# Kernel tuning notes

Hardware: AMD Instinct MI355X
Metric: run time of the kernel (lower is better)

## Reference

```python
import jax, jax.numpy as jnp
import numpy as np

H, D = 16, 1024
HD = D // H  # 64

def setup_inputs() -> dict:
    key = jax.random.key(0)
    ks = jax.random.split(key, 11)
    B, S = 2, 2048
    s_in = 1.0 / np.sqrt(D)
    return {
        "V": jax.random.normal(ks[0], (B, S, D), jnp.float32),
        "K": jax.random.normal(ks[1], (B, S, D), jnp.float32),
        "Q": jax.random.normal(ks[2], (B, S, D), jnp.float32),
        # stacked per-head Linear weights, torch layout [out,in] -> [H, HD, D]
        "Wv": jax.random.normal(ks[3], (H, HD, D), jnp.float32) * s_in,
        "bv": jnp.zeros((H, HD), jnp.float32),
        "Wk": jax.random.normal(ks[4], (H, HD, D), jnp.float32) * s_in,
        "bk": jnp.zeros((H, HD), jnp.float32),
        "Wq": jax.random.normal(ks[5], (H, HD, D), jnp.float32) * s_in,
        "bq": jnp.zeros((H, HD), jnp.float32),
        "Wo": jax.random.normal(ks[6], (D, D), jnp.float32) * s_in,
        "bo": jnp.zeros((D,), jnp.float32),
    }

def reference(V, K, Q, Wv, bv, Wk, bk, Wq, bq, Wo, bo):
    scale = HD ** (-0.5)
    # per-head projections fused into one batched GEMM: [B,S,D] x [H,HD,D] -> [B,H,S,HD]
    q = jnp.einsum('bsd,hed->bhse', Q, Wq) + bq[None, :, None, :]
    k = jnp.einsum('bsd,hed->bhse', K, Wk) + bk[None, :, None, :]
    v = jnp.einsum('bsd,hed->bhse', V, Wv) + bv[None, :, None, :]
    # scaled dot-product attention
    scores = jnp.einsum('bhqe,bhke->bhqk', q, k) * scale  # [B,H,S,S]
    p = jax.nn.softmax(scores, axis=-1)
    att = jnp.einsum('bhqk,bhke->bhqe', p, v)  # [B,H,S,HD]
    # concat heads (head 0 first, matching the torch cat order) then output proj
    B, _, S, _ = att.shape
    cat = jnp.transpose(att, (0, 2, 1, 3)).reshape(B, S, H * HD)
    return cat @ Wo.T + bo
```

## Files before the change

kernel.cpp:

```cpp
#include <hip/hip_runtime.h>
#include <cstdint>
#include <cstddef>

typedef __bf16 bf16_t;
typedef bf16_t bf16x8 __attribute__((ext_vector_type(8)));
typedef bf16_t bf16x4 __attribute__((ext_vector_type(4)));
typedef float f32x4 __attribute__((ext_vector_type(4)));

__device__ __forceinline__ void gl_lds16(const void* g, void* l) {
  __builtin_amdgcn_global_load_lds(
      (const __attribute__((address_space(1))) void*)g,
      (__attribute__((address_space(3))) void*)l, 16, 0, 0);
}

__device__ __forceinline__ f32x4 mfma16(bf16x8 a, bf16x8 b, f32x4 c) {
  return __builtin_amdgcn_mfma_f32_16x16x32_bf16(a, b, c, 0, 0, 0);
}

#define SCHED_FENCE() __builtin_amdgcn_sched_barrier(0)
#define WAIT_VM0()   do { asm volatile("s_waitcnt vmcnt(0)");   SCHED_FENCE(); } while (0)
#define WAIT_LGKM0() do { asm volatile("s_waitcnt lgkmcnt(0)"); SCHED_FENCE(); } while (0)
#define RAW_BAR()    do { __builtin_amdgcn_s_barrier();         SCHED_FENCE(); } while (0)

struct CvtArgs { const float* src[7]; bf16_t* dst[7]; };

__global__ __launch_bounds__(256) void convert_all(CvtArgs a) {
  unsigned g = blockIdx.x * 256u + threadIdx.x;
  unsigned seg, off;
  if (g < 524288u) {
    seg = g >> 17; off = g & 131071u;
  } else {
    unsigned h = g - 524288u;
    seg = 4u + (h >> 19); off = h & 524287u;
  }
  const float4* s = (const float4*)a.src[seg] + (size_t)off * 2;
  float4 x0 = s[0], x1 = s[1];
  bf16x8 o;
  o[0] = (bf16_t)x0.x; o[1] = (bf16_t)x0.y; o[2] = (bf16_t)x0.z; o[3] = (bf16_t)x0.w;
  o[4] = (bf16_t)x1.x; o[5] = (bf16_t)x1.y; o[6] = (bf16_t)x1.z; o[7] = (bf16_t)x1.w;
  *(bf16x8*)(a.dst[seg] + (size_t)off * 8) = o;
}

__device__ __forceinline__ void stage128(const bf16_t* src, bf16_t* dst, int t, int w) {
  #pragma unroll
  for (int i = 0; i < 4; i++) {
    int g = t + i * 256;
    int r = g >> 3, pc = g & 7;
    int lc = pc ^ (r & 7);
    gl_lds16(src + (size_t)r * 1024 + lc * 8, dst + i * 2048 + w * 512);
  }
}
__device__ __forceinline__ void stage64(const bf16_t* src, bf16_t* dst, int t, int w) {
  #pragma unroll
  for (int i = 0; i < 2; i++) {
    int g = t + i * 256;
    int r = g >> 3, pc = g & 7;
    int lc = pc ^ (r & 7);
    gl_lds16(src + (size_t)r * 1024 + lc * 8, dst + i * 2048 + w * 512);
  }
}

struct ProjArgs {
  const bf16_t* A[3]; const bf16_t* W[3]; const float* bias[3];
  bf16_t* out[3]; float scale[3];
};

__global__ __launch_bounds__(256, 2) void gemm_proj(ProjArgs p) {
  __shared__ __attribute__((aligned(16))) unsigned char smem[65536];
  const int z = blockIdx.z;
  const bf16_t* A = p.A[z] + (size_t)blockIdx.x * 128 * 1024;
  const bf16_t* W = p.W[z] + (size_t)blockIdx.y * 128 * 1024;

  const int t = threadIdx.x;
  const int w = t >> 6, l = t & 63;
  const int lq = l >> 4, lr = l & 15;
  const int mq = w & 1, nq = w >> 1;

  f32x4 acc[4][4];
  f32x4 zero = {0.f, 0.f, 0.f, 0.f};
  #pragma unroll
  for (int i = 0; i < 4; i++)
    #pragma unroll
    for (int j = 0; j < 4; j++) acc[i][j] = zero;

  stage128(A, (bf16_t*)smem, t, w);
  stage128(W, (bf16_t*)(smem + 16384), t, w);
  WAIT_VM0();
  RAW_BAR();

  for (int step = 0; step < 16; ++step) {
    const int cur = step & 1;
    bf16_t* as = (bf16_t*)(smem + cur * 32768);
    bf16_t* bs = (bf16_t*)(smem + cur * 32768 + 16384);
    if (step < 15) {
      bf16_t* an = (bf16_t*)(smem + (cur ^ 1) * 32768);
      stage128(A + (step + 1) * 64, an, t, w);
      stage128(W + (step + 1) * 64, an + 8192, t, w);
    }
    SCHED_FENCE();
    #pragma unroll
    for (int kk = 0; kk < 2; kk++) {
      bf16x8 af[4], bfr[4];
      #pragma unroll
      for (int i = 0; i < 4; i++) {
        int R = mq * 64 + i * 16 + lr;
        int ch = (kk * 4 + lq) ^ (R & 7);
        af[i] = *(const bf16x8*)(as + R * 64 + ch * 8);
      }
      #pragma unroll
      for (int j = 0; j < 4; j++) {
        int R = nq * 64 + j * 16 + lr;
        int ch = (kk * 4 + lq) ^ (R & 7);
        bfr[j] = *(const bf16x8*)(bs + R * 64 + ch * 8);
      }
      __builtin_amdgcn_s_setprio(1);
      #pragma unroll
      for (int i = 0; i < 4; i++)
        #pragma unroll
        for (int j = 0; j < 4; j++)
          acc[i][j] = mfma16(af[i], bfr[j], acc[i][j]);
      __builtin_amdgcn_s_setprio(0);
    }
    WAIT_VM0();
    RAW_BAR();
  }

  const float* bias = p.bias[z];
  const float scale = p.scale[z];
  __syncthreads();
  bf16_t* ts = (bf16_t*)smem;
  #pragma unroll
  for (int i = 0; i < 4; i++) {
    #pragma unroll
    for (int j = 0; j < 4; j++) {
      int nl = nq * 64 + j * 16 + lr;
      float bz = bias[blockIdx.y * 128 + nl];
      #pragma unroll
      for (int r = 0; r < 4; r++) {
        int ml = mq * 64 + i * 16 + lq * 4 + r;
        bf16_t val = (bf16_t)((acc[i][j][r] + bz) * scale);
        if (z == 0) {
          int mlp = (ml & 96) | (((ml >> 2) & 3) << 3) | (((ml >> 4) & 1) << 2) | (ml & 3);
          ts[nl * 136 + mlp] = val;
        } else {
          ts[ml * 136 + nl] = val;
        }
      }
    }
  }
  __syncthreads();
  bf16_t* out = p.out[z];
  const int b = blockIdx.x >> 4, sbase = (blockIdx.x & 15) * 128;
  if (z == 0) {
    #pragma unroll
    for (int ii = 0; ii < 8; ii++) {
      int idx = t * 8 + ii * 2048;
      int rr = idx >> 7, cc = idx & 127;
      int n = blockIdx.y * 128 + rr;
      int h = n >> 6, e = n & 63;
      bf16x8 vq = *(const bf16x8*)(ts + rr * 136 + cc);
      *(bf16x8*)(out + ((size_t)(b * 16 + h) * 64 + e) * 2048 + sbase + cc) = vq;
    }
  } else {
    #pragma unroll
    for (int ii = 0; ii < 8; ii++) {
      int idx = t * 8 + ii * 2048;
      int rr = idx >> 7, cc = idx & 127;
      int n = blockIdx.y * 128 + cc;
      int h = n >> 6, e = n & 63;
      bf16x8 vq = *(const bf16x8*)(ts + rr * 136 + cc);
      *(bf16x8*)(out + ((size_t)(b * 16 + h) * 2048 + sbase + rr) * 64 + e) = vq;
    }
  }
}

__global__ __launch_bounds__(256, 4) void attn(
    const bf16_t* __restrict__ qw, const bf16_t* __restrict__ kw,
    const bf16_t* __restrict__ vtw, bf16_t* __restrict__ att)
{
  __shared__ __attribute__((aligned(16))) unsigned char smem[32768];
  bf16_t* qe_s = (bf16_t*)(smem + 16384);
  const int bh = blockIdx.x, qt = blockIdx.y;
  const int t = threadIdx.x, w = t >> 6, l = t & 63, lq = l >> 4, lr = l & 15;

  const bf16_t* kb0 = kw + (size_t)bh * 131072;
  const bf16_t* vb0 = vtw + (size_t)bh * 131072;

  const bf16_t* qbase = qw + ((size_t)bh * 2048 + qt * 64) * 64;
  #pragma unroll
  for (int i = 0; i < 2; i++) {
    int g = t + i * 256;
    int r = g >> 3, pc = g & 7;
    int lc = pc ^ (r & 7);
    gl_lds16(qbase + (size_t)r * 64 + lc * 8, qe_s + i * 2048 + w * 512);
    gl_lds16(kb0 + (size_t)r * 64 + lc * 8, (bf16_t*)smem + i * 2048 + w * 512);
    gl_lds16(vb0 + (size_t)r * 2048 + lc * 8, (bf16_t*)(smem + 8192) + i * 2048 + w * 512);
  }
  WAIT_VM0();
  RAW_BAR();
  bf16x8 qf[2];
  #pragma unroll
  for (int kk = 0; kk < 2; kk++) {
    int R = w * 16 + lr;
    int ch = (kk * 4 + lq) ^ (R & 7);
    qf[kk] = *(const bf16x8*)(qe_s + R * 64 + ch * 8);
  }
  WAIT_LGKM0();
  RAW_BAR();

  f32x4 O[4];
  f32x4 zero = {0.f, 0.f, 0.f, 0.f};
  #pragma unroll
  for (int et = 0; et < 4; et++) O[et] = zero;
  float lsum = 0.f;

  for (int kt = 0; kt < 32; ++kt) {
    const int cur = kt & 1;
    bf16_t* ks = (bf16_t*)(smem + cur * 16384);
    bf16_t* vs = (bf16_t*)(smem + cur * 16384 + 8192);
    if (kt < 31) {
      bf16_t* kn = (bf16_t*)(smem + (cur ^ 1) * 16384);
      const bf16_t* kbase = kb0 + (size_t)(kt + 1) * 64 * 64;
      const bf16_t* vbase = vb0 + (size_t)(kt + 1) * 64;
      #pragma unroll
      for (int i = 0; i < 2; i++) {
        int g = t + i * 256;
        int r = g >> 3, pc = g & 7;
        int lc = pc ^ (r & 7);
        gl_lds16(kbase + (size_t)r * 64 + lc * 8, kn + i * 2048 + w * 512);
        gl_lds16(vbase + (size_t)r * 2048 + lc * 8, kn + 4096 + i * 2048 + w * 512);
      }
    }
    SCHED_FENCE();

    f32x4 sc[4];
    #pragma unroll
    for (int j = 0; j < 4; j++) sc[j] = zero;
    #pragma unroll
    for (int kk = 0; kk < 2; kk++) {
      #pragma unroll
      for (int j = 0; j < 4; j++) {
        int R = j * 16 + lr;
        int ch = (kk * 4 + lq) ^ (R & 7);
        bf16x8 kf = *(const bf16x8*)(ks + R * 64 + ch * 8);
        __builtin_amdgcn_s_setprio(1);
        sc[j] = mfma16(kf, qf[kk], sc[j]);
        __builtin_amdgcn_s_setprio(0);
      }
    }

    bf16x8 pb[2];
    #pragma unroll
    for (int ks2 = 0; ks2 < 2; ks2++) {
      #pragma unroll
      for (int r = 0; r < 4; r++) {
        float e0 = __expf(sc[2 * ks2][r]);
        float e1 = __expf(sc[2 * ks2 + 1][r]);
        lsum += e0 + e1;
        pb[ks2][r] = (bf16_t)e0;
        pb[ks2][4 + r] = (bf16_t)e1;
      }
    }

    #pragma unroll
    for (int ks2 = 0; ks2 < 2; ks2++) {
      #pragma unroll
      for (int et = 0; et < 4; et++) {
        int R = et * 16 + lr;
        int ch = (ks2 * 4 + lq) ^ (R & 7);
        bf16x8 vf = *(const bf16x8*)(vs + R * 64 + ch * 8);
        __builtin_amdgcn_s_setprio(1);
        O[et] = mfma16(vf, pb[ks2], O[et]);
        __builtin_amdgcn_s_setprio(0);
      }
    }
    WAIT_VM0();
    RAW_BAR();
  }

  float s = lsum;
  s += __shfl_xor(s, 16);
  s += __shfl_xor(s, 32);
  float rinv = 1.0f / s;

  #pragma unroll
  for (int et = 0; et < 4; et++) {
    bf16x4 pv;
    #pragma unroll
    for (int r = 0; r < 4; r++) pv[r] = (bf16_t)(O[et][r] * rinv);
    *(bf16x4*)(qe_s + (w * 16 + lr) * 72 + et * 16 + lq * 4) = pv;
  }
  __syncthreads();
  const int b = bh >> 4, h = bh & 15;
  #pragma unroll
  for (int i = 0; i < 2; i++) {
    int c = t + i * 256;
    int row = c >> 3, c8 = c & 7;
    bf16x8 vv = *(const bf16x8*)(qe_s + row * 72 + c8 * 8);
    *(bf16x8*)(att + ((size_t)b * 2048 + qt * 64 + row) * 1024 + h * 64 + c8 * 8) = vv;
  }
}

__global__ __launch_bounds__(256, 3) void gemm_out(
    const bf16_t* __restrict__ A, const bf16_t* __restrict__ W,
    const float* __restrict__ bias, float* __restrict__ out)
{
  __shared__ __attribute__((aligned(16))) unsigned char smem[49152];
  const bf16_t* Ab = A + (size_t)blockIdx.x * 64 * 1024;
  const bf16_t* Wb = W + (size_t)blockIdx.y * 128 * 1024;
  const int t = threadIdx.x, w = t >> 6, l = t & 63, lq = l >> 4, lr = l & 15;
  const int mh = w & 1, nh = w >> 1;

  f32x4 acc[2][4];
  f32x4 zero = {0.f, 0.f, 0.f, 0.f};
  #pragma unroll
  for (int i = 0; i < 2; i++)
    #pragma unroll
    for (int j = 0; j < 4; j++) acc[i][j] = zero;

  stage64(Ab, (bf16_t*)smem, t, w);
  stage128(Wb, (bf16_t*)(smem + 8192), t, w);
  WAIT_VM0();
  RAW_BAR();

  for (int step = 0; step < 16; ++step) {
    const int cur = step & 1;
    bf16_t* as = (bf16_t*)(smem + cur * 24576);
    bf16_t* bs = (bf16_t*)(smem + cur * 24576 + 8192);
    if (step < 15) {
      bf16_t* an = (bf16_t*)(smem + (cur ^ 1) * 24576);
      stage64(Ab + (step + 1) * 64, an, t, w);
      stage128(Wb + (step + 1) * 64, an + 4096, t, w);
    }
    SCHED_FENCE();
    #pragma unroll
    for (int kk = 0; kk < 2; kk++) {
      bf16x8 af[2], bfr[4];
      #pragma unroll
      for (int i = 0; i < 2; i++) {
        int R = mh * 32 + i * 16 + lr;
        int ch = (kk * 4 + lq) ^ (R & 7);
        af[i] = *(const bf16x8*)(as + R * 64 + ch * 8);
      }
      #pragma unroll
      for (int j = 0; j < 4; j++) {
        int R = nh * 64 + j * 16 + lr;
        int ch = (kk * 4 + lq) ^ (R & 7);
        bfr[j] = *(const bf16x8*)(bs + R * 64 + ch * 8);
      }
      __builtin_amdgcn_s_setprio(1);
      #pragma unroll
      for (int i = 0; i < 2; i++)
        #pragma unroll
        for (int j = 0; j < 4; j++)
          acc[i][j] = mfma16(af[i], bfr[j], acc[i][j]);
      __builtin_amdgcn_s_setprio(0);
    }
    WAIT_VM0();
    RAW_BAR();
  }

  #pragma unroll
  for (int i = 0; i < 2; i++) {
    #pragma unroll
    for (int j = 0; j < 4; j++) {
      int col = blockIdx.y * 128 + nh * 64 + j * 16 + lr;
      float bz = bias[col];
      #pragma unroll
      for (int r = 0; r < 4; r++) {
        int row = blockIdx.x * 64 + mh * 32 + i * 16 + lq * 4 + r;
        out[(size_t)row * 1024 + col] = acc[i][j][r] + bz;
      }
    }
  }
}

extern "C" void kernel_launch(void* const* d_in, const int* in_sizes, int n_in,
                              void* d_out, int out_size, void* d_ws, size_t ws_size,
                              hipStream_t stream) {
  (void)in_sizes; (void)n_in; (void)out_size;
  const float* V  = (const float*)d_in[0];
  const float* Kx = (const float*)d_in[1];
  const float* Q  = (const float*)d_in[2];
  const float* Wv = (const float*)d_in[3];
  const float* bv = (const float*)d_in[4];
  const float* Wk = (const float*)d_in[5];
  const float* bk = (const float*)d_in[6];
  const float* Wq = (const float*)d_in[7];
  const float* bq = (const float*)d_in[8];
  const float* Wo = (const float*)d_in[9];
  const float* bo = (const float*)d_in[10];

  const size_t E = 1048576;
  if (ws_size < 20 * E * sizeof(bf16_t)) return;

  bf16_t* ws = (bf16_t*)d_ws;
  bf16_t* cWo   = ws;
  bf16_t* cWv   = ws + E;
  bf16_t* cWk   = ws + 2 * E;
  bf16_t* cWq   = ws + 3 * E;
  bf16_t* q_ws  = ws + 4 * E;
  bf16_t* k_ws  = ws + 8 * E;
  bf16_t* vt_ws = ws + 12 * E;
  bf16_t* att_ws= ws + 16 * E;

  bf16_t* cV = att_ws;
  bf16_t* cK = (bf16_t*)d_out;
  bf16_t* cQ = (bf16_t*)d_out + 4 * E;

  CvtArgs ca;
  ca.src[0] = Wo; ca.src[1] = Wv; ca.src[2] = Wk; ca.src[3] = Wq;
  ca.src[4] = V;  ca.src[5] = Kx; ca.src[6] = Q;
  ca.dst[0] = cWo; ca.dst[1] = cWv; ca.dst[2] = cWk; ca.dst[3] = cWq;
  ca.dst[4] = cV;  ca.dst[5] = cK;  ca.dst[6] = cQ;
  convert_all<<<8192, 256, 0, stream>>>(ca);

  ProjArgs pa;
  pa.A[0] = cV;  pa.A[1] = cK;  pa.A[2] = cQ;
  pa.W[0] = cWv; pa.W[1] = cWk; pa.W[2] = cWq;
  pa.bias[0] = bv; pa.bias[1] = bk; pa.bias[2] = bq;
  pa.out[0] = vt_ws; pa.out[1] = k_ws; pa.out[2] = q_ws;
  pa.scale[0] = 1.f; pa.scale[1] = 1.f; pa.scale[2] = 0.125f;
  gemm_proj<<<dim3(32, 8, 3), 256, 0, stream>>>(pa);

  attn<<<dim3(32, 32), 256, 0, stream>>>(q_ws, k_ws, vt_ws, att_ws);

  gemm_out<<<dim3(64, 8), 256, 0, stream>>>(att_ws, cWo, bo, (float*)d_out);
}
```

Baseline: 207.4 us.

## Software-pipeline attention PV MFMA across iterations and use native exp2

Restructures the attention loop so each iteration's P·V MFMAs use the probabilities and V fragments from the previous tile, interleaved with the current QK^T MFMAs. V fragments are preloaded into registers. The intent is to hide the exp/softmax latency and LDS reads behind matrix work. The log2(e) factor is folded into the Q projection scale so a raw v_exp_f32 replaces __expf, and the row sum accumulates as a packed float2. The cost is more register pressure from holding 8 V fragments and two P buffers, which could reduce occupancy.

```diff
diff --git a/kernel.cpp b/kernel.cpp
--- a/kernel.cpp
+++ b/kernel.cpp
@@ -6,6 +6,7 @@
 typedef bf16_t bf16x8 __attribute__((ext_vector_type(8)));
 typedef bf16_t bf16x4 __attribute__((ext_vector_type(4)));
 typedef float f32x4 __attribute__((ext_vector_type(4)));
+typedef float f32x2 __attribute__((ext_vector_type(2)));
 
 __device__ __forceinline__ void gl_lds16(const void* g, void* l) {
   __builtin_amdgcn_global_load_lds(
@@ -15,6 +16,12 @@
 
 __device__ __forceinline__ f32x4 mfma16(bf16x8 a, bf16x8 b, f32x4 c) {
   return __builtin_amdgcn_mfma_f32_16x16x32_bf16(a, b, c, 0, 0, 0);
+}
+
+__device__ __forceinline__ float exp2_fast(float x) {
+  float r;
+  asm("v_exp_f32 %0, %1" : "=v"(r) : "v"(x));
+  return r;
 }
 
 #define SCHED_FENCE() __builtin_amdgcn_sched_barrier(0)
@@ -212,73 +219,88 @@
   f32x4 zero = {0.f, 0.f, 0.f, 0.f};
   #pragma unroll
   for (int et = 0; et < 4; et++) O[et] = zero;
-  float lsum = 0.f;
-
-  for (int kt = 0; kt < 32; ++kt) {
-    const int cur = kt & 1;
-    bf16_t* ks = (bf16_t*)(smem + cur * 16384);
-    bf16_t* vs = (bf16_t*)(smem + cur * 16384 + 8192);
-    if (kt < 31) {
-      bf16_t* kn = (bf16_t*)(smem + (cur ^ 1) * 16384);
-      const bf16_t* kbase = kb0 + (size_t)(kt + 1) * 64 * 64;
-      const bf16_t* vbase = vb0 + (size_t)(kt + 1) * 64;
-      #pragma unroll
-      for (int i = 0; i < 2; i++) {
-        int g = t + i * 256;
-        int r = g >> 3, pc = g & 7;
-        int lc = pc ^ (r & 7);
-        gl_lds16(kbase + (size_t)r * 64 + lc * 8, kn + i * 2048 + w * 512);
-        gl_lds16(vbase + (size_t)r * 2048 + lc * 8, kn + 4096 + i * 2048 + w * 512);
-      }
-    }
-    SCHED_FENCE();
-
-    f32x4 sc[4];
-    #pragma unroll
-    for (int j = 0; j < 4; j++) sc[j] = zero;
-    #pragma unroll
-    for (int kk = 0; kk < 2; kk++) {
-      #pragma unroll
-      for (int j = 0; j < 4; j++) {
-        int R = j * 16 + lr;
-        int ch = (kk * 4 + lq) ^ (R & 7);
-        bf16x8 kf = *(const bf16x8*)(ks + R * 64 + ch * 8);
-        __builtin_amdgcn_s_setprio(1);
-        sc[j] = mfma16(kf, qf[kk], sc[j]);
-        __builtin_amdgcn_s_setprio(0);
-      }
-    }
-
-    bf16x8 pb[2];
-    #pragma unroll
-    for (int ks2 = 0; ks2 < 2; ks2++) {
-      #pragma unroll
-      for (int r = 0; r < 4; r++) {
-        float e0 = __expf(sc[2 * ks2][r]);
-        float e1 = __expf(sc[2 * ks2 + 1][r]);
-        lsum += e0 + e1;
-        pb[ks2][r] = (bf16_t)e0;
-        pb[ks2][4 + r] = (bf16_t)e1;
-      }
-    }
-
-    #pragma unroll
-    for (int ks2 = 0; ks2 < 2; ks2++) {
-      #pragma unroll
-      for (int et = 0; et < 4; et++) {
-        int R = et * 16 + lr;
-        int ch = (ks2 * 4 + lq) ^ (R & 7);
-        bf16x8 vf = *(const bf16x8*)(vs + R * 64 + ch * 8);
-        __builtin_amdgcn_s_setprio(1);
-        O[et] = mfma16(vf, pb[ks2], O[et]);
-        __builtin_amdgcn_s_setprio(0);
-      }
-    }
-    WAIT_VM0();
-    RAW_BAR();
-  }
-
-  float s = lsum;
+  f32x2 ls = {0.f, 0.f};
+  bf16x8 vf[8];
+  bf16x8 pbA[2], pbB[2];
+
+#define ATTN_BODY(KT, CUR, PBOUT, PBIN, FIRST, DOSTAGE)                          \
+  {                                                                              \
+    bf16_t* ksb = (bf16_t*)(smem + (CUR) * 16384);                               \
+    bf16_t* vsb = (bf16_t*)(smem + (CUR) * 16384 + 8192);                        \
+    if (DOSTAGE) {                                                               \
+      bf16_t* kn = (bf16_t*)(smem + ((CUR) ^ 1) * 16384);                        \
+      const bf16_t* kbase = kb0 + (size_t)((KT) + 1) * 4096;                     \
+      const bf16_t* vbase = vb0 + (size_t)((KT) + 1) * 64;                       \
+      _Pragma("unroll")                                                          \
+      for (int i = 0; i < 2; i++) {                                              \
+        int g = t + i * 256;                                                     \
+        int r = g >> 3, pc = g & 7;                                              \
+        int lc = pc ^ (r & 7);                                                   \
+        gl_lds16(kbase + (size_t)r * 64 + lc * 8, kn + i * 2048 + w * 512);      \
+        gl_lds16(vbase + (size_t)r * 2048 + lc * 8, kn + 4096 + i * 2048 + w * 512); \
+      }                                                                          \
+    }                                                                            \
+    f32x4 sc[4];                                                                 \
+    _Pragma("unroll")                                                            \
+    for (int j = 0; j < 4; j++) sc[j] = zero;                                    \
+    __builtin_amdgcn_s_setprio(1);                                               \
+    if (!(FIRST)) {                                                              \
+      _Pragma("unroll")                                                          \
+      for (int ks2 = 0; ks2 < 2; ks2++)                                          \
+        _Pragma("unroll")                                                        \
+        for (int et = 0; et < 4; et++)                                           \
+          O[et] = mfma16(vf[ks2 * 4 + et], (PBIN)[ks2], O[et]);                  \
+    }                                                                            \
+    _Pragma("unroll")                                                            \
+    for (int kk = 0; kk < 2; kk++)                                               \
+      _Pragma("unroll")                                                          \
+      for (int j = 0; j < 4; j++) {                                              \
+        int R = j * 16 + lr;                                                     \
+        int ch = (kk * 4 + lq) ^ (R & 7);                                        \
+        bf16x8 kf = *(const bf16x8*)(ksb + R * 64 + ch * 8);                     \
+        sc[j] = mfma16(kf, qf[kk], sc[j]);                                       \
+      }                                                                          \
+    __builtin_amdgcn_s_setprio(0);                                               \
+    _Pragma("unroll")                                                            \
+    for (int ks2 = 0; ks2 < 2; ks2++)                                            \
+      _Pragma("unroll")                                                          \
+      for (int et = 0; et < 4; et++) {                                           \
+        int R = et * 16 + lr;                                                    \
+        int ch = (ks2 * 4 + lq) ^ (R & 7);                                       \
+        vf[ks2 * 4 + et] = *(const bf16x8*)(vsb + R * 64 + ch * 8);              \
+      }                                                                          \
+    _Pragma("unroll")                                                            \
+    for (int ks2 = 0; ks2 < 2; ks2++)                                            \
+      _Pragma("unroll")                                                          \
+      for (int r = 0; r < 4; r++) {                                              \
+        float e0 = exp2_fast(sc[2 * ks2][r]);                                    \
+        float e1 = exp2_fast(sc[2 * ks2 + 1][r]);                                \
+        f32x2 ee = {e0, e1};                                                     \
+        ls += ee;                                                                \
+        (PBOUT)[ks2][r] = (bf16_t)e0;                                            \
+        (PBOUT)[ks2][4 + r] = (bf16_t)e1;                                        \
+      }                                                                          \
+    WAIT_LGKM0();         \
+    if (DOSTAGE) WAIT_VM0();                             \
+    RAW_BAR();                                                                   \
+  }
+
+  ATTN_BODY(0, 0, pbA, pbB, true, true);
+  ATTN_BODY(1, 1, pbB, pbA, false, true);
+  for (int kt2 = 1; kt2 < 16; ++kt2) {
+    const int kt = kt2 * 2;
+    ATTN_BODY(kt, 0, pbA, pbB, false, true);
+    ATTN_BODY(kt + 1, 1, pbB, pbA, false, (kt2 < 15));
+  }
+#undef ATTN_BODY
+
+  #pragma unroll
+  for (int ks2 = 0; ks2 < 2; ks2++)
+    #pragma unroll
+    for (int et = 0; et < 4; et++)
+      O[et] = mfma16(vf[ks2 * 4 + et], pbB[ks2], O[et]);
+
+  float s = ls[0] + ls[1];
   s += __shfl_xor(s, 16);
   s += __shfl_xor(s, 32);
   float rinv = 1.0f / s;
@@ -420,7 +442,7 @@
   pa.W[0] = cWv; pa.W[1] = cWk; pa.W[2] = cWq;
   pa.bias[0] = bv; pa.bias[1] = bk; pa.bias[2] = bq;
   pa.out[0] = vt_ws; pa.out[1] = k_ws; pa.out[2] = q_ws;
-  pa.scale[0] = 1.f; pa.scale[1] = 1.f; pa.scale[2] = 0.125f;
+  pa.scale[0] = 1.f; pa.scale[1] = 1.f; pa.scale[2] = 0.125f * 1.4426950408889634f;
   gemm_proj<<<dim3(32, 8, 3), 256, 0, stream>>>(pa);
 
   attn<<<dim3(32, 32), 256, 0, stream>>>(q_ws, k_ws, vt_ws, att_ws);
```

New measurement: 205.4 us. No clear change (-0.9%).

## Enlarge attention tiles to 128 queries and 128 keys with exp2 softmax

Applied to the files above, without the earlier changes.

The attention kernel now handles 128 query rows per block (32 per wave, two MFMA row groups), so each K/V fragment loaded from LDS feeds two MFMAs. Key tiles grow from 64 to 128 keys, which halves the number of loop iterations and barriers. The ln2 factor is folded into the Q scale so the softmax can use the raw v_exp_f32 instruction, and PV MFMAs are interleaved with exponent computation per key chunk. In exchange LDS use doubles to 64KB and register pressure rises, so occupancy drops (launch bounds go from 4 to 2) and the grid has half as many blocks. Softmax still has no max subtraction, the same as before.

```diff
diff --git a/kernel.cpp b/kernel.cpp
--- a/kernel.cpp
+++ b/kernel.cpp
@@ -6,6 +6,7 @@
 typedef bf16_t bf16x8 __attribute__((ext_vector_type(8)));
 typedef bf16_t bf16x4 __attribute__((ext_vector_type(4)));
 typedef float f32x4 __attribute__((ext_vector_type(4)));
+typedef float f32x2 __attribute__((ext_vector_type(2)));
 
 __device__ __forceinline__ void gl_lds16(const void* g, void* l) {
   __builtin_amdgcn_global_load_lds(
@@ -15,6 +16,12 @@
 
 __device__ __forceinline__ f32x4 mfma16(bf16x8 a, bf16x8 b, f32x4 c) {
   return __builtin_amdgcn_mfma_f32_16x16x32_bf16(a, b, c, 0, 0, 0);
+}
+
+__device__ __forceinline__ float exp2_fast(float x) {
+  float r;
+  asm("v_exp_f32 %0, %1" : "=v"(r) : "v"(x));
+  return r;
 }
 
 #define SCHED_FENCE() __builtin_amdgcn_sched_barrier(0)
@@ -174,130 +181,170 @@
   }
 }
 
-__global__ __launch_bounds__(256, 4) void attn(
+__global__ __launch_bounds__(256, 2) void attn(
     const bf16_t* __restrict__ qw, const bf16_t* __restrict__ kw,
     const bf16_t* __restrict__ vtw, bf16_t* __restrict__ att)
 {
-  __shared__ __attribute__((aligned(16))) unsigned char smem[32768];
-  bf16_t* qe_s = (bf16_t*)(smem + 16384);
+  __shared__ __attribute__((aligned(16))) unsigned char smem[65536];
   const int bh = blockIdx.x, qt = blockIdx.y;
   const int t = threadIdx.x, w = t >> 6, l = t & 63, lq = l >> 4, lr = l & 15;
 
   const bf16_t* kb0 = kw + (size_t)bh * 131072;
   const bf16_t* vb0 = vtw + (size_t)bh * 131072;
-
-  const bf16_t* qbase = qw + ((size_t)bh * 2048 + qt * 64) * 64;
-  #pragma unroll
-  for (int i = 0; i < 2; i++) {
+  bf16_t* qstage = (bf16_t*)(smem + 32768);
+
+  const bf16_t* qbase = qw + ((size_t)bh * 2048 + qt * 128) * 64;
+  #pragma unroll
+  for (int i = 0; i < 4; i++) {
     int g = t + i * 256;
     int r = g >> 3, pc = g & 7;
     int lc = pc ^ (r & 7);
-    gl_lds16(qbase + (size_t)r * 64 + lc * 8, qe_s + i * 2048 + w * 512);
+    gl_lds16(qbase + (size_t)r * 64 + lc * 8, qstage + i * 2048 + w * 512);
+  }
+  #pragma unroll
+  for (int i = 0; i < 4; i++) {
+    int g = t + i * 256;
+    int r = g >> 3, pc = g & 7;
+    int lc = pc ^ (r & 7);
     gl_lds16(kb0 + (size_t)r * 64 + lc * 8, (bf16_t*)smem + i * 2048 + w * 512);
-    gl_lds16(vb0 + (size_t)r * 2048 + lc * 8, (bf16_t*)(smem + 8192) + i * 2048 + w * 512);
-  }
-  WAIT_VM0();
+  }
+  #pragma unroll
+  for (int i = 0; i < 4; i++) {
+    int g = t + i * 256;
+    int r = g >> 4, c16 = g & 15;
+    int lc = c16 ^ (r & 7);
+    gl_lds16(vb0 + (size_t)r * 2048 + lc * 8, (bf16_t*)(smem + 16384) + i * 2048 + w * 512);
+  }
+  asm volatile("s_waitcnt vmcnt(8)");
+  SCHED_FENCE();
   RAW_BAR();
-  bf16x8 qf[2];
-  #pragma unroll
-  for (int kk = 0; kk < 2; kk++) {
-    int R = w * 16 + lr;
-    int ch = (kk * 4 + lq) ^ (R & 7);
-    qf[kk] = *(const bf16x8*)(qe_s + R * 64 + ch * 8);
-  }
-  WAIT_LGKM0();
+  bf16x8 qf[2][2];
+  #pragma unroll
+  for (int gq = 0; gq < 2; gq++)
+    #pragma unroll
+    for (int kk = 0; kk < 2; kk++) {
+      int R = w * 32 + gq * 16 + lr;
+      int ch = (kk * 4 + lq) ^ (R & 7);
+      qf[gq][kk] = *(const bf16x8*)(qstage + R * 64 + ch * 8);
+    }
+  asm volatile("s_waitcnt vmcnt(0) lgkmcnt(0)");
+  SCHED_FENCE();
   RAW_BAR();
 
-  f32x4 O[4];
+  f32x4 O[2][4];
   f32x4 zero = {0.f, 0.f, 0.f, 0.f};
   #pragma unroll
-  for (int et = 0; et < 4; et++) O[et] = zero;
-  float lsum = 0.f;
-
-  for (int kt = 0; kt < 32; ++kt) {
+  for (int gq = 0; gq < 2; gq++)
+    #pragma unroll
+    for (int et = 0; et < 4; et++) O[gq][et] = zero;
+  f32x2 lsv[2];
+  lsv[0] = f32x2{0.f, 0.f}; lsv[1] = f32x2{0.f, 0.f};
+
+  for (int kt = 0; kt < 16; ++kt) {
     const int cur = kt & 1;
-    bf16_t* ks = (bf16_t*)(smem + cur * 16384);
-    bf16_t* vs = (bf16_t*)(smem + cur * 16384 + 8192);
-    if (kt < 31) {
-      bf16_t* kn = (bf16_t*)(smem + (cur ^ 1) * 16384);
-      const bf16_t* kbase = kb0 + (size_t)(kt + 1) * 64 * 64;
-      const bf16_t* vbase = vb0 + (size_t)(kt + 1) * 64;
-      #pragma unroll
-      for (int i = 0; i < 2; i++) {
+    bf16_t* ksb = (bf16_t*)(smem + cur * 32768);
+    bf16_t* vsb = (bf16_t*)(smem + cur * 32768 + 16384);
+    if (kt < 15) {
+      bf16_t* kn = (bf16_t*)(smem + (cur ^ 1) * 32768);
+      const bf16_t* kbase = kb0 + (size_t)(kt + 1) * 8192;
+      const bf16_t* vbase = vb0 + (size_t)(kt + 1) * 128;
+      #pragma unroll
+      for (int i = 0; i < 4; i++) {
         int g = t + i * 256;
         int r = g >> 3, pc = g & 7;
         int lc = pc ^ (r & 7);
         gl_lds16(kbase + (size_t)r * 64 + lc * 8, kn + i * 2048 + w * 512);
-        gl_lds16(vbase + (size_t)r * 2048 + lc * 8, kn + 4096 + i * 2048 + w * 512);
+      }
+      #pragma unroll
+      for (int i = 0; i < 4; i++) {
+        int g = t + i * 256;
+        int r = g >> 4, c16 = g & 15;
+        int lc = c16 ^ (r & 7);
+        gl_lds16(vbase + (size_t)r * 2048 + lc * 8, kn + 8192 + i * 2048 + w * 512);
       }
     }
     SCHED_FENCE();
 
-    f32x4 sc[4];
-    #pragma unroll
-    for (int j = 0; j < 4; j++) sc[j] = zero;
-    #pragma unroll
-    for (int kk = 0; kk < 2; kk++) {
-      #pragma unroll
-      for (int j = 0; j < 4; j++) {
+    f32x4 sc[2][8];
+    #pragma unroll
+    for (int gq = 0; gq < 2; gq++)
+      #pragma unroll
+      for (int j = 0; j < 8; j++) sc[gq][j] = zero;
+    __builtin_amdgcn_s_setprio(1);
+    #pragma unroll
+    for (int kk = 0; kk < 2; kk++)
+      #pragma unroll
+      for (int j = 0; j < 8; j++) {
         int R = j * 16 + lr;
         int ch = (kk * 4 + lq) ^ (R & 7);
-        bf16x8 kf = *(const bf16x8*)(ks + R * 64 + ch * 8);
-        __builtin_amdgcn_s_setprio(1);
-        sc[j] = mfma16(kf, qf[kk], sc[j]);
-        __builtin_amdgcn_s_setprio(0);
-      }
-    }
-
-    bf16x8 pb[2];
-    #pragma unroll
-    for (int ks2 = 0; ks2 < 2; ks2++) {
+        bf16x8 kf = *(const bf16x8*)(ksb + R * 64 + ch * 8);
+        sc[0][j] = mfma16(kf, qf[0][kk], sc[0][j]);
+        sc[1][j] = mfma16(kf, qf[1][kk], sc[1][j]);
+      }
+    __builtin_amdgcn_s_setprio(0);
+
+    #pragma unroll
+    for (int ks2 = 0; ks2 < 4; ks2++) {
+      bf16x8 pb0, pb1;
       #pragma unroll
       for (int r = 0; r < 4; r++) {
-        float e0 = __expf(sc[2 * ks2][r]);
-        float e1 = __expf(sc[2 * ks2 + 1][r]);
-        lsum += e0 + e1;
-        pb[ks2][r] = (bf16_t)e0;
-        pb[ks2][4 + r] = (bf16_t)e1;
-      }
-    }
-
-    #pragma unroll
-    for (int ks2 = 0; ks2 < 2; ks2++) {
+        float e00 = exp2_fast(sc[0][2 * ks2][r]);
+        float e01 = exp2_fast(sc[0][2 * ks2 + 1][r]);
+        float e10 = exp2_fast(sc[1][2 * ks2][r]);
+        float e11 = exp2_fast(sc[1][2 * ks2 + 1][r]);
+        f32x2 ee0 = {e00, e01}, ee1 = {e10, e11};
+        lsv[0] += ee0; lsv[1] += ee1;
+        pb0[r] = (bf16_t)e00; pb0[4 + r] = (bf16_t)e01;
+        pb1[r] = (bf16_t)e10; pb1[4 + r] = (bf16_t)e11;
+      }
+      bf16x8 vf[4];
       #pragma unroll
       for (int et = 0; et < 4; et++) {
         int R = et * 16 + lr;
-        int ch = (ks2 * 4 + lq) ^ (R & 7);
-        bf16x8 vf = *(const bf16x8*)(vs + R * 64 + ch * 8);
-        __builtin_amdgcn_s_setprio(1);
-        O[et] = mfma16(vf, pb[ks2], O[et]);
-        __builtin_amdgcn_s_setprio(0);
-      }
-    }
-    WAIT_VM0();
+        int cc = ks2 * 4 + lq;
+        int ph = cc ^ (R & 7);
+        vf[et] = *(const bf16x8*)(vsb + R * 128 + ph * 8);
+      }
+      __builtin_amdgcn_s_setprio(1);
+      #pragma unroll
+      for (int et = 0; et < 4; et++) {
+        O[0][et] = mfma16(vf[et], pb0, O[0][et]);
+        O[1][et] = mfma16(vf[et], pb1, O[1][et]);
+      }
+      __builtin_amdgcn_s_setprio(0);
+    }
+
+    asm volatile("s_waitcnt vmcnt(0) lgkmcnt(0)");
+    SCHED_FENCE();
     RAW_BAR();
   }
 
-  float s = lsum;
-  s += __shfl_xor(s, 16);
-  s += __shfl_xor(s, 32);
-  float rinv = 1.0f / s;
-
-  #pragma unroll
-  for (int et = 0; et < 4; et++) {
-    bf16x4 pv;
-    #pragma unroll
-    for (int r = 0; r < 4; r++) pv[r] = (bf16_t)(O[et][r] * rinv);
-    *(bf16x4*)(qe_s + (w * 16 + lr) * 72 + et * 16 + lq * 4) = pv;
-  }
+  float s0 = lsv[0][0] + lsv[0][1];
+  float s1 = lsv[1][0] + lsv[1][1];
+  s0 += __shfl_xor(s0, 16);
+  s0 += __shfl_xor(s0, 32);
+  s1 += __shfl_xor(s1, 16);
+  s1 += __shfl_xor(s1, 32);
+  float rinv[2] = {1.0f / s0, 1.0f / s1};
+
+  bf16_t* ts = (bf16_t*)smem;
+  #pragma unroll
+  for (int gq = 0; gq < 2; gq++)
+    #pragma unroll
+    for (int et = 0; et < 4; et++) {
+      bf16x4 pv;
+      #pragma unroll
+      for (int r = 0; r < 4; r++) pv[r] = (bf16_t)(O[gq][et][r] * rinv[gq]);
+      *(bf16x4*)(ts + (w * 32 + gq * 16 + lr) * 72 + et * 16 + lq * 4) = pv;
+    }
   __syncthreads();
   const int b = bh >> 4, h = bh & 15;
   #pragma unroll
-  for (int i = 0; i < 2; i++) {
+  for (int i = 0; i < 4; i++) {
     int c = t + i * 256;
     int row = c >> 3, c8 = c & 7;
-    bf16x8 vv = *(const bf16x8*)(qe_s + row * 72 + c8 * 8);
-    *(bf16x8*)(att + ((size_t)b * 2048 + qt * 64 + row) * 1024 + h * 64 + c8 * 8) = vv;
+    bf16x8 vv = *(const bf16x8*)(ts + row * 72 + c8 * 8);
+    *(bf16x8*)(att + ((size_t)b * 2048 + qt * 128 + row) * 1024 + h * 64 + c8 * 8) = vv;
   }
 }
 
@@ -420,10 +467,10 @@
   pa.W[0] = cWv; pa.W[1] = cWk; pa.W[2] = cWq;
   pa.bias[0] = bv; pa.bias[1] = bk; pa.bias[2] = bq;
   pa.out[0] = vt_ws; pa.out[1] = k_ws; pa.out[2] = q_ws;
-  pa.scale[0] = 1.f; pa.scale[1] = 1.f; pa.scale[2] = 0.125f;
+  pa.scale[0] = 1.f; pa.scale[1] = 1.f; pa.scale[2] = 0.125f * 1.4426950408889634f;
   gemm_proj<<<dim3(32, 8, 3), 256, 0, stream>>>(pa);
 
-  attn<<<dim3(32, 32), 256, 0, stream>>>(q_ws, k_ws, vt_ws, att_ws);
+  attn<<<dim3(32, 16), 256, 0, stream>>>(q_ws, k_ws, vt_ws, att_ws);
 
   gemm_out<<<dim3(64, 8), 256, 0, stream>>>(att_ws, cWo, bo, (float*)d_out);
 }
```

New measurement: 200.3 us. -3.4%, faster.
